# Optimization experiments

Measured on AMD Instinct MI355X. Metric: run time of the kernel, lower is better.

Reference implementation:

```python
import jax, jax.numpy as jnp
import numpy as np

B, N, C, NT = 32, 512, 32, 24   # batch, frames, channels-per-token, tokens
H, DH = 8, 48                   # heads, dim_head (DH % NT == 0 -> CS = 2)
E = H * DH                      # encode_dim = 384
IN = C * NT                     # in_dim = 768
OUT = 768                       # out_dim


def setup_inputs() -> dict:
    key = jax.random.key(0)
    ks = jax.random.split(key, 12)
    s = lambda fan_in: 1.0 / np.sqrt(fan_in)
    return {
        "x": jax.random.normal(ks[0], (B, N, C, NT), dtype=jnp.float32),
        "Wqkv_t": jax.random.uniform(ks[1], (IN, 3 * E), jnp.float32, -s(IN), s(IN)),
        "bqkv_t": jax.random.uniform(ks[2], (3 * E,), jnp.float32, -s(IN), s(IN)),
        "Wqkv_s": jax.random.uniform(ks[3], (IN, 3 * E), jnp.float32, -s(IN), s(IN)),
        "bqkv_s": jax.random.uniform(ks[4], (3 * E,), jnp.float32, -s(IN), s(IN)),
        "Wts": jax.random.uniform(ks[5], (2 * E, 2 * E), jnp.float32, -s(2 * E), s(2 * E)),
        "bts": jax.random.uniform(ks[6], (2 * E,), jnp.float32, -s(2 * E), s(2 * E)),
        "Wfc_t": jax.random.uniform(ks[7], (E, OUT), jnp.float32, -s(E), s(E)),
        "bfc_t": jax.random.uniform(ks[8], (OUT,), jnp.float32, -s(E), s(E)),
        "Wfc_s": jax.random.uniform(ks[9], (E, OUT), jnp.float32, -s(E), s(E)),
        "bfc_s": jax.random.uniform(ks[10], (OUT,), jnp.float32, -s(E), s(E)),
    }


def reference(x, Wqkv_t, bqkv_t, Wqkv_s, bqkv_s, Wts, bts, Wfc_t, bfc_t, Wfc_s, bfc_s):
    b, n, c, nt = x.shape
    cs = DH // nt  # channels per token inside a head (=2)
    xf = x.reshape(b, n, c * nt)                       # (b, n, in_dim)

    # --- temporal attention over the n (frame) axis ---
    qkv_t = (xf @ Wqkv_t + bqkv_t).reshape(b, n, 3, H, DH)
    qkv_t = jnp.transpose(qkv_t, (2, 0, 3, 1, 4))      # (3, b, H, n, DH)
    qt, kt, vt = qkv_t[0], qkv_t[1], qkv_t[2]
    attn_t = jax.nn.softmax(
        jnp.einsum('bhnd,bhmd->bhnm', qt, kt) / jnp.sqrt(jnp.float32(DH)), axis=-1)
    x_t = jnp.einsum('bhnm,bhmd->bnhd', attn_t, vt).reshape(b, n, E)

    # --- spatial attention over the nt (token) axis (note: unscaled, per source) ---
    qkv_s = (xf @ Wqkv_s + bqkv_s).reshape(b, n, 3, H, DH)
    qkv_s = jnp.transpose(qkv_s, (2, 0, 1, 3, 4)).reshape(3, b * n, H, cs, nt)
    qs, ks_, vs = qkv_s[0], qkv_s[1], qkv_s[2]         # (b*n, H, cs, nt)
    attn_s = jax.nn.softmax(jnp.einsum('ghct,ghcu->ghtu', qs, ks_), axis=-1)
    x_s = jnp.einsum('ghtu,ghcu->ghct', attn_s, vs)     # (b*n, H, cs, nt)
    x_s = x_s.reshape(b * n, H, cs * nt).reshape(b, n, E)

    # --- learned gating fusion ---
    alpha = jnp.concatenate([x_t, x_s], axis=-1).mean(axis=1, keepdims=True)  # (b,1,2E)
    alpha = (alpha @ Wts + bts).reshape(b, 1, E, 2)
    alpha = jax.nn.softmax(alpha, axis=-1)
    y = (x_t * alpha[:, :, :, 0]) @ Wfc_t + bfc_t + (x_s * alpha[:, :, :, 1]) @ Wfc_s + bfc_s
    return y  # dropout is identity in inference
```

## Files before the change

### kernel.cpp

```cpp
#include <hip/hip_runtime.h>
#include <hip/hip_bf16.h>


typedef __attribute__((ext_vector_type(8))) short s16x8;
typedef __attribute__((ext_vector_type(4))) float f32x4;

__device__ __forceinline__ float lo2f(uint u) { return __uint_as_float(u << 16); }
__device__ __forceinline__ float hi2f(uint u) { return __uint_as_float(u & 0xffff0000u); }
__device__ __forceinline__ ushort f2bu(float f) {
    union { __hip_bfloat16 h; ushort u; } c; c.h = __float2bfloat16(f); return c.u;
}
__device__ __forceinline__ uint pk2(float a, float b) {
    return (uint)f2bu(a) | ((uint)f2bu(b) << 16);
}
__device__ __forceinline__ void gload16(const void* g, void* l) {
    __builtin_amdgcn_global_load_lds((const __attribute__((address_space(1))) void*)g,
                                     (__attribute__((address_space(3))) void*)l, 16, 0, 0);
}

__global__ __launch_bounds__(256) void convert_bf16(
    const float* __restrict__ in, ushort* __restrict__ out)
{
    const int i = blockIdx.x * 256 + threadIdx.x;
    const float4* p = (const float4*)in + (size_t)i * 2;
    float4 a = p[0], b = p[1];
    uint4 o;
    o.x = pk2(a.x, a.y); o.y = pk2(a.z, a.w);
    o.z = pk2(b.x, b.y); o.w = pk2(b.z, b.w);
    ((uint4*)out)[i] = o;
}

__global__ __launch_bounds__(256) void concat_bias(
    const float* __restrict__ a, const float* __restrict__ b, float* __restrict__ o)
{
    const int i = blockIdx.x * 256 + threadIdx.x;
    o[i] = (i < 1152) ? a[i] : b[i - 1152];
}

__global__ __launch_bounds__(256) void transpose_w(
    const float* __restrict__ W, ushort* __restrict__ Bt,
    int K, int N, int Kt, int koff, int noff)
{
    __shared__ float t[32][33];
    const int k0 = blockIdx.x * 32, n0 = blockIdx.y * 32;
    const int r = threadIdx.x >> 3, cq = threadIdx.x & 7;
    float4 v = *(const float4*)(W + (size_t)(k0 + r) * N + n0 + cq * 4);
    t[r][cq * 4 + 0] = v.x; t[r][cq * 4 + 1] = v.y;
    t[r][cq * 4 + 2] = v.z; t[r][cq * 4 + 3] = v.w;
    __syncthreads();
    ushort4 o;
    o.x = f2bu(t[cq * 4 + 0][r]); o.y = f2bu(t[cq * 4 + 1][r]);
    o.z = f2bu(t[cq * 4 + 2][r]); o.w = f2bu(t[cq * 4 + 3][r]);
    *(ushort4*)(Bt + (size_t)(noff + n0 + r) * Kt + koff + k0 + cq * 4) = o;
}

template<int OUTBF16, int NBIAS>
__global__ __launch_bounds__(256, 2) void gemm128p(
    const ushort* __restrict__ A, const ushort* __restrict__ Bt,
    const float* __restrict__ bias0, const float* __restrict__ bias1,
    void* __restrict__ Cout, int M, int N, int K)
{
    __shared__ ushort smem[32768];
    const int tid = threadIdx.x;
    const int m0 = blockIdx.x * 128;
    const int n0 = blockIdx.y * 128;
    const int lane = tid & 63;
    const int wr = tid >> 7;
    const int wc = (tid >> 6) & 1;
    const int lr = lane & 15;
    const int g = lane >> 4;

    f32x4 acc[4][4];
#pragma unroll
    for (int i = 0; i < 4; ++i)
#pragma unroll
        for (int j = 0; j < 4; ++j) acc[i][j] = (f32x4){0.f, 0.f, 0.f, 0.f};

    int rowT[4], kqs[4];
#pragma unroll
    for (int i = 0; i < 4; ++i) {
        const int task = tid + 256 * i;
        rowT[i] = task >> 3;
        kqs[i] = (task & 7) ^ (rowT[i] & 7);
    }

    auto stage = [&](int buf, int k0) {
        ushort* dA = &smem[buf * 16384];
        ushort* dB = &smem[buf * 16384 + 8192];
#pragma unroll
        for (int i = 0; i < 4; ++i) {
            gload16(A + (size_t)(m0 + rowT[i]) * K + k0 + (kqs[i] << 3),
                    dA + (tid + 256 * i) * 8);
            gload16(Bt + (size_t)(n0 + rowT[i]) * K + k0 + (kqs[i] << 3),
                    dB + (tid + 256 * i) * 8);
        }
    };

    stage(0, 0);
    const int nt = K >> 6;
    for (int t = 0; t < nt; ++t) {
        const int cur = t & 1;
        if (t + 1 < nt) {
            stage(cur ^ 1, (t + 1) << 6);
            asm volatile("s_waitcnt vmcnt(8)" ::: "memory");
        } else {
            asm volatile("s_waitcnt vmcnt(0)" ::: "memory");
        }
        __builtin_amdgcn_sched_barrier(0);
        __builtin_amdgcn_s_barrier();
        __builtin_amdgcn_sched_barrier(0);

        const ushort* As = &smem[cur * 16384];
        const ushort* Bs = &smem[cur * 16384 + 8192];
#pragma unroll
        for (int half = 0; half < 2; ++half) {
            s16x8 af[4], bfv[4];
#pragma unroll
            for (int i = 0; i < 4; ++i) {
                const int row = wr * 64 + 16 * i + lr;
                af[i] = *(const s16x8*)&As[row * 64
                         + (((4 * half + g) ^ (row & 7)) << 3)];
            }
#pragma unroll
            for (int j = 0; j < 4; ++j) {
                const int row = wc * 64 + 16 * j + lr;
                bfv[j] = *(const s16x8*)&Bs[row * 64
                          + (((4 * half + g) ^ (row & 7)) << 3)];
            }
#pragma unroll
            for (int i = 0; i < 4; ++i)
#pragma unroll
                for (int j = 0; j < 4; ++j)
                    acc[i][j] = __builtin_amdgcn_mfma_f32_16x16x32_bf16(
                        af[i], bfv[j], acc[i][j], 0, 0, 0);
        }
        __builtin_amdgcn_sched_barrier(0);
        __builtin_amdgcn_s_barrier();
    }

    const int c0 = n0 + wc * 64 + lr;
    float bsum[4];
#pragma unroll
    for (int j = 0; j < 4; ++j) {
        bsum[j] = bias0[c0 + 16 * j];
        if (NBIAS == 2) bsum[j] += bias1[c0 + 16 * j];
    }
    const int r0 = m0 + wr * 64 + g * 4;
#pragma unroll
    for (int i = 0; i < 4; ++i) {
        const int row = r0 + 16 * i;
#pragma unroll
        for (int j = 0; j < 4; ++j) {
            const int col = c0 + 16 * j;
#pragma unroll
            for (int v = 0; v < 4; ++v) {
                const float val = acc[i][j][v] + bsum[j];
                if (OUTBF16)
                    ((ushort*)Cout)[(size_t)(row + v) * N + col] = f2bu(val);
                else
                    ((float*)Cout)[(size_t)(row + v) * N + col] = val;
            }
        }
    }
}

__global__ __launch_bounds__(256, 4) void attn_temporal(
    const ushort* __restrict__ qkv, ushort* __restrict__ xcat)
{
    const int wg = blockIdx.x;
    const int cx = wg & 7, rx = wg >> 3;
    const int id = ((rx >> 2) << 5) + 4 * cx + (rx & 3);
    const int qt = id & 3;
    const int h = (id >> 2) & 7;
    const int b = id >> 5;

    const int tid = threadIdx.x;
    const int w = tid >> 6;
    const int lane = tid & 63;
    const int lr = lane & 15;
    const int g = lane >> 4;

    __shared__ ushort Ks[64 * 64];
    __shared__ ushort Vt[48 * 64];
    __shared__ ushort Pl[4][32 * 72];
    uint* KsU = (uint*)Ks;
    uint* VtU = (uint*)Vt;

    ((uint4*)Ks)[tid] = make_uint4(0u, 0u, 0u, 0u);
    ((uint4*)Ks)[256 + tid] = make_uint4(0u, 0u, 0u, 0u);
    __syncthreads();

    const uint* qkvu = (const uint*)qkv;
    const int qrow0 = qt * 128 + w * 32;

    s16x8 qf[2][2];
#pragma unroll
    for (int n = 0; n < 2; ++n) {
        const size_t rb = (size_t)(b * 512 + qrow0 + 16 * n + lr) * 2304 + h * 48 + 8 * g;
        qf[n][0] = *(const s16x8*)(qkv + rb);
        qf[n][1] = (g < 2) ? *(const s16x8*)(qkv + rb + 32)
                           : (s16x8){0, 0, 0, 0, 0, 0, 0, 0};
    }

    int p_[3], du_[3];
#pragma unroll
    for (int i = 0; i < 3; ++i) {
        const int idx = tid + 256 * i;
        p_[i] = idx / 24;
        du_[i] = idx % 24;
    }
    uint rk[3][2], rv[3][2];

    auto stage_load = [&](int kv0) {
#pragma unroll
        for (int i = 0; i < 3; ++i) {
            const uint* s0 = qkvu + (size_t)(b * 512 + kv0 + 2 * p_[i]) * 1152
                                  + 192 + h * 24 + du_[i];
            rk[i][0] = s0[0];    rk[i][1] = s0[1152];
            rv[i][0] = s0[192];  rv[i][1] = s0[192 + 1152];
        }
    };
    auto stage_write = [&]() {
#pragma unroll
        for (int i = 0; i < 3; ++i) {
            const int p = p_[i], du = du_[i];
            KsU[(2 * p) * 32 + ((((du >> 2) ^ ((2 * p) & 7)) << 2) | (du & 3))] = rk[i][0];
            KsU[(2 * p + 1) * 32 + ((((du >> 2) ^ ((2 * p + 1) & 7)) << 2) | (du & 3))] = rk[i][1];
            const uint w0 = (rv[i][0] & 0xffffu) | (rv[i][1] << 16);
            const uint w1 = (rv[i][0] >> 16) | (rv[i][1] & 0xffff0000u);
            const int vb = (((p >> 2) ^ (du & 7)) << 2) | (p & 3);
            VtU[(2 * du) * 32 + vb] = w0;
            VtU[(2 * du + 1) * 32 + vb] = w1;
        }
    };

    f32x4 o[2][3];
#pragma unroll
    for (int mq = 0; mq < 2; ++mq)
#pragma unroll
        for (int nd = 0; nd < 3; ++nd) o[mq][nd] = (f32x4){0.f, 0.f, 0.f, 0.f};
    float mrun[2] = {-3.0e38f, -3.0e38f};
    float lsum[2] = {0.f, 0.f};
    float corrv[2];
    const float scale = 0.14433756729740643f;

    stage_load(0);
    stage_write();
    __syncthreads();

    for (int t = 0; t < 8; ++t) {
        if (t < 7) stage_load((t + 1) * 64);

        f32x4 sa[4][2];
#pragma unroll
        for (int m = 0; m < 4; ++m)
#pragma unroll
            for (int n = 0; n < 2; ++n) sa[m][n] = (f32x4){0.f, 0.f, 0.f, 0.f};
#pragma unroll
        for (int ks = 0; ks < 2; ++ks)
#pragma unroll
            for (int m = 0; m < 4; ++m) {
                s16x8 kf = *(const s16x8*)&Ks[(16 * m + lr) * 64
                                              + (((g + 4 * ks) ^ (lr & 7)) << 3)];
#pragma unroll
                for (int n = 0; n < 2; ++n)
                    sa[m][n] = __builtin_amdgcn_mfma_f32_16x16x32_bf16(
                        kf, qf[n][ks], sa[m][n], 0, 0, 0);
            }

#pragma unroll
        for (int n = 0; n < 2; ++n) {
            float tmax = -3.0e38f;
#pragma unroll
            for (int m = 0; m < 4; ++m)
#pragma unroll
                for (int v = 0; v < 4; ++v) tmax = fmaxf(tmax, sa[m][n][v]);
            tmax = fmaxf(tmax, __shfl_xor(tmax, 16));
            tmax = fmaxf(tmax, __shfl_xor(tmax, 32));
            float mnew = fmaxf(mrun[n], tmax * scale);
            float corr = __expf(mrun[n] - mnew);
            mrun[n] = mnew;
            float psum = 0.f;
#pragma unroll
            for (int m = 0; m < 4; ++m) {
                float p0 = __expf(fmaf(sa[m][n][0], scale, -mnew));
                float p1 = __expf(fmaf(sa[m][n][1], scale, -mnew));
                float p2 = __expf(fmaf(sa[m][n][2], scale, -mnew));
                float p3 = __expf(fmaf(sa[m][n][3], scale, -mnew));
                psum += (p0 + p1) + (p2 + p3);
                const int base = (16 * n + lr) * 72 + 16 * m + 4 * g;
                *(uint*)&Pl[w][base] = pk2(p0, p1);
                *(uint*)&Pl[w][base + 2] = pk2(p2, p3);
            }
            psum += __shfl_xor(psum, 16);
            psum += __shfl_xor(psum, 32);
            lsum[n] = lsum[n] * corr + psum;
            corrv[n] = corr;
        }

#pragma unroll
        for (int mq = 0; mq < 2; ++mq)
#pragma unroll
            for (int nd = 0; nd < 3; ++nd)
#pragma unroll
                for (int v = 0; v < 4; ++v) o[mq][nd][v] *= corrv[mq];

#pragma unroll
        for (int ks = 0; ks < 2; ++ks) {
            s16x8 vf[3];
#pragma unroll
            for (int nd = 0; nd < 3; ++nd)
                vf[nd] = *(const s16x8*)&Vt[(16 * nd + lr) * 64
                                            + (((g + 4 * ks) ^ (lr >> 1)) << 3)];
#pragma unroll
            for (int mq = 0; mq < 2; ++mq) {
                s16x8 pf = *(const s16x8*)&Pl[w][(16 * mq + lr) * 72 + 8 * g + 32 * ks];
#pragma unroll
                for (int nd = 0; nd < 3; ++nd)
                    o[mq][nd] = __builtin_amdgcn_mfma_f32_16x16x32_bf16(
                        vf[nd], pf, o[mq][nd], 0, 0, 0);
            }
        }
        __syncthreads();
        if (t < 7) stage_write();
        __syncthreads();
    }

#pragma unroll
    for (int mq = 0; mq < 2; ++mq) {
        const float li = 1.f / lsum[mq];
        const int qrow = qrow0 + 16 * mq + lr;
        ushort* dst = xcat + (size_t)(b * 512 + qrow) * 768 + h * 48;
#pragma unroll
        for (int nd = 0; nd < 3; ++nd) {
            uint2 o2;
            o2.x = pk2(o[mq][nd][0] * li, o[mq][nd][1] * li);
            o2.y = pk2(o[mq][nd][2] * li, o[mq][nd][3] * li);
            *(uint2*)(dst + 16 * nd + 4 * g) = o2;
        }
    }
}

__global__ __launch_bounds__(192) void attn_spatial(
    const ushort* __restrict__ qkv, ushort* __restrict__ xcat)
{
    const int g = blockIdx.x;
    __shared__ float row[1152];
    const uint* qkvu = (const uint*)qkv;
#pragma unroll
    for (int i = 0; i < 3; ++i) {
        int idx = threadIdx.x + 192 * i;
        uint u = qkvu[(size_t)g * 1152 + 576 + idx];
        row[2 * idx] = lo2f(u); row[2 * idx + 1] = hi2f(u);
    }
    __syncthreads();

    const int h = threadIdx.x / 24;
    const int t = threadIdx.x % 24;
    const float* q = &row[h * 48];
    const float* k = &row[384 + h * 48];
    const float* v = &row[768 + h * 48];
    const float q0 = q[t], q1 = q[24 + t];

    float s[24];
    float mx = -3.0e38f;
#pragma unroll
    for (int u = 0; u < 24; ++u) {
        s[u] = q0 * k[u] + q1 * k[24 + u];
        mx = fmaxf(mx, s[u]);
    }
    float l = 0.f;
#pragma unroll
    for (int u = 0; u < 24; ++u) { s[u] = __expf(s[u] - mx); l += s[u]; }
    const float inv = 1.f / l;
    float o0 = 0.f, o1 = 0.f;
#pragma unroll
    for (int u = 0; u < 24; ++u) {
        o0 = fmaf(s[u], v[u], o0);
        o1 = fmaf(s[u], v[24 + u], o1);
    }
    ushort* dst = xcat + (size_t)g * 768 + 384 + h * 48;
    dst[t] = f2bu(o0 * inv);
    dst[24 + t] = f2bu(o1 * inv);
}

__global__ __launch_bounds__(256) void colsum(
    const ushort* __restrict__ xcat, float* __restrict__ partial)
{
    const int b = blockIdx.x, ch = blockIdx.y, part = blockIdx.z;
    const int e = ch * 256 + threadIdx.x;
    const int n0 = part * 64;
    float s = 0.f;
    for (int n = 0; n < 64; ++n)
        s += __uint_as_float((uint)xcat[((size_t)(b * 512 + n0 + n)) * 768 + e] << 16);
    partial[((size_t)(b * 8 + part)) * 768 + e] = s;
}

__global__ __launch_bounds__(256) void alpha_gate(
    const float* __restrict__ partial, const float* __restrict__ Wts,
    const float* __restrict__ bts, float* __restrict__ gate)
{
    const int b = blockIdx.x;
    const int j0 = blockIdx.y * 128;
    __shared__ float av[768];
    __shared__ float psum[2][128];

    for (int i = threadIdx.x; i < 768; i += 256) {
        float s = 0.f;
#pragma unroll
        for (int p = 0; p < 8; ++p)
            s += partial[((size_t)(b * 8 + p)) * 768 + i];
        av[i] = s * (1.0f / 512.0f);
    }
    __syncthreads();

    const int jl = threadIdx.x & 127;
    const int seg = threadIdx.x >> 7;
    const int j = j0 + jl;
    const float* Wp = Wts + (size_t)(seg * 384) * 768 + j;
    const float* avp = av + seg * 384;
    float a0 = 0.f, a1 = 0.f, a2 = 0.f, a3 = 0.f;
    float a4 = 0.f, a5 = 0.f, a6 = 0.f, a7 = 0.f;
#pragma unroll 4
    for (int k = 0; k < 384; k += 8) {
        a0 = fmaf(avp[k + 0], Wp[(size_t)(k + 0) * 768], a0);
        a1 = fmaf(avp[k + 1], Wp[(size_t)(k + 1) * 768], a1);
        a2 = fmaf(avp[k + 2], Wp[(size_t)(k + 2) * 768], a2);
        a3 = fmaf(avp[k + 3], Wp[(size_t)(k + 3) * 768], a3);
        a4 = fmaf(avp[k + 4], Wp[(size_t)(k + 4) * 768], a4);
        a5 = fmaf(avp[k + 5], Wp[(size_t)(k + 5) * 768], a5);
        a6 = fmaf(avp[k + 6], Wp[(size_t)(k + 6) * 768], a6);
        a7 = fmaf(avp[k + 7], Wp[(size_t)(k + 7) * 768], a7);
    }
    psum[seg][jl] = ((a0 + a1) + (a2 + a3)) + ((a4 + a5) + (a6 + a7));
    __syncthreads();

    if (threadIdx.x < 128)
        av[threadIdx.x] = psum[0][threadIdx.x] + psum[1][threadIdx.x]
                        + bts[j0 + threadIdx.x];
    __syncthreads();
    if (threadIdx.x < 64) {
        const int e = (j0 >> 1) + threadIdx.x;
        float x0 = av[2 * threadIdx.x], x1 = av[2 * threadIdx.x + 1];
        float m = fmaxf(x0, x1);
        float e0 = __expf(x0 - m), e1 = __expf(x1 - m);
        float inv = 1.f / (e0 + e1);
        gate[(size_t)b * 768 + e] = e0 * inv;
        gate[(size_t)b * 768 + 384 + e] = e1 * inv;
    }
}

__global__ __launch_bounds__(256) void gate_mul(
    const ushort* __restrict__ xcat, const float* __restrict__ gate,
    ushort* __restrict__ xg)
{
    const int i = blockIdx.x * 256 + threadIdx.x;
    const int m = i / 96;
    const int k = (i % 96) * 8;
    const int b = m >> 9;
    uint4 u = ((const uint4*)xcat)[i];
    const float* g = gate + (size_t)b * 768 + k;
    float4 g0 = *(const float4*)g;
    float4 g1 = *(const float4*)(g + 4);
    uint4 o;
    o.x = pk2(lo2f(u.x) * g0.x, hi2f(u.x) * g0.y);
    o.y = pk2(lo2f(u.y) * g0.z, hi2f(u.y) * g0.w);
    o.z = pk2(lo2f(u.z) * g1.x, hi2f(u.z) * g1.y);
    o.w = pk2(lo2f(u.w) * g1.z, hi2f(u.w) * g1.w);
    ((uint4*)xg)[i] = o;
}

extern "C" void kernel_launch(void* const* d_in, const int* in_sizes, int n_in,
                              void* d_out, int out_size, void* d_ws, size_t ws_size,
                              hipStream_t stream)
{
    const float* x      = (const float*)d_in[0];
    const float* Wqkv_t = (const float*)d_in[1];
    const float* bqkv_t = (const float*)d_in[2];
    const float* Wqkv_s = (const float*)d_in[3];
    const float* bqkv_s = (const float*)d_in[4];
    const float* Wts    = (const float*)d_in[5];
    const float* bts    = (const float*)d_in[6];
    const float* Wfc_t  = (const float*)d_in[7];
    const float* bfc_t  = (const float*)d_in[8];
    const float* Wfc_s  = (const float*)d_in[9];
    const float* bfc_s  = (const float*)d_in[10];
    float* out = (float*)d_out;

    char* w = (char*)d_ws;
    ushort* qkv2   = (ushort*)(w);
    ushort* xg     = qkv2;
    ushort* xcat   = (ushort*)(w + 75497472);
    ushort* xb     = (ushort*)(w + 100663296);
    ushort* wbuf   = (ushort*)(w + 125829120);
    ushort* wbuf2  = (ushort*)(w + 129368064);
    float*  partial= (float*)(w + 130547712);
    float*  gate   = (float*)(w + 131334144);
    float*  bias2  = (float*)(w + 131432448);

    const dim3 blk256(256);

    convert_bf16<<<dim3(6144), blk256, 0, stream>>>(x, xb);
    concat_bias<<<dim3(9), blk256, 0, stream>>>(bqkv_t, bqkv_s, bias2);
    transpose_w<<<dim3(24, 36), blk256, 0, stream>>>(Wqkv_t, wbuf, 768, 1152, 768, 0, 0);
    transpose_w<<<dim3(24, 36), blk256, 0, stream>>>(Wqkv_s, wbuf, 768, 1152, 768, 0, 1152);

    gemm128p<1, 1><<<dim3(128, 18), blk256, 0, stream>>>(
        xb, wbuf, bias2, nullptr, qkv2, 16384, 2304, 768);

    attn_temporal<<<dim3(1024), blk256, 0, stream>>>(qkv2, xcat);
    attn_spatial<<<dim3(16384), dim3(192), 0, stream>>>(qkv2, xcat);

    colsum<<<dim3(32, 3, 8), blk256, 0, stream>>>(xcat, partial);
    alpha_gate<<<dim3(32, 6), blk256, 0, stream>>>(partial, Wts, bts, gate);
    gate_mul<<<dim3(6144), blk256, 0, stream>>>(xcat, gate, xg);

    transpose_w<<<dim3(12, 24), blk256, 0, stream>>>(Wfc_t, wbuf2, 384, 768, 768, 0, 0);
    transpose_w<<<dim3(12, 24), blk256, 0, stream>>>(Wfc_s, wbuf2, 384, 768, 768, 384, 0);
    gemm128p<0, 2><<<dim3(128, 6), blk256, 0, stream>>>(
        xg, wbuf2, bfc_t, bfc_s, out, 16384, 768, 768);
}
```

Measured before the change: 200.5 us.

## Enlarge GEMM tiles to 256x256 with 512 threads and XCD-aware block mapping

Replaces the 128x128 GEMM with a 256x256 tile using 8 waves (each computing 128x64) and 64KB of double-buffered LDS. It also remaps the 1D grid so that each XCD gets a contiguous range of M row-blocks, which should improve L2 reuse of A. The goal is higher arithmetic intensity per LDS load and fewer global reloads. The cost is fewer blocks (576 and 192 on 256 CUs, giving wave-quantization imbalance) and higher register pressure from 32 accumulators per wave, with only one block per CU.

```diff
diff --git a/kernel.cpp b/kernel.cpp
--- a/kernel.cpp
+++ b/kernel.cpp
@@ -54,45 +54,51 @@
     *(ushort4*)(Bt + (size_t)(noff + n0 + r) * Kt + koff + k0 + cq * 4) = o;
 }
 
-template<int OUTBF16, int NBIAS>
-__global__ __launch_bounds__(256, 2) void gemm128p(
+template<int OUTBF16, int NBIAS, int NBT>
+__global__ __launch_bounds__(512, 1) void gemm256p(
     const ushort* __restrict__ A, const ushort* __restrict__ Bt,
     const float* __restrict__ bias0, const float* __restrict__ bias1,
     void* __restrict__ Cout, int M, int N, int K)
 {
-    __shared__ ushort smem[32768];
+    __shared__ ushort smem[65536];
     const int tid = threadIdx.x;
-    const int m0 = blockIdx.x * 128;
-    const int n0 = blockIdx.y * 128;
+
+    const int id = blockIdx.x;
+    const int xcd = id & 7;
+    const int j = id >> 3;
+    const int m0 = (xcd * ((M >> 8) >> 3) + j / NBT) << 8;
+    const int n0 = (j % NBT) << 8;
+
     const int lane = tid & 63;
-    const int wr = tid >> 7;
-    const int wc = (tid >> 6) & 1;
+    const int wid = tid >> 6;
+    const int wr = wid >> 2;
+    const int wc = wid & 3;
     const int lr = lane & 15;
     const int g = lane >> 4;
 
-    f32x4 acc[4][4];
-#pragma unroll
-    for (int i = 0; i < 4; ++i)
-#pragma unroll
-        for (int j = 0; j < 4; ++j) acc[i][j] = (f32x4){0.f, 0.f, 0.f, 0.f};
+    f32x4 acc[8][4];
+#pragma unroll
+    for (int i = 0; i < 8; ++i)
+#pragma unroll
+        for (int jj = 0; jj < 4; ++jj) acc[i][jj] = (f32x4){0.f, 0.f, 0.f, 0.f};
 
     int rowT[4], kqs[4];
 #pragma unroll
     for (int i = 0; i < 4; ++i) {
-        const int task = tid + 256 * i;
+        const int task = tid + 512 * i;
         rowT[i] = task >> 3;
         kqs[i] = (task & 7) ^ (rowT[i] & 7);
     }
 
     auto stage = [&](int buf, int k0) {
-        ushort* dA = &smem[buf * 16384];
-        ushort* dB = &smem[buf * 16384 + 8192];
+        ushort* dA = &smem[buf * 32768];
+        ushort* dB = &smem[buf * 32768 + 16384];
 #pragma unroll
         for (int i = 0; i < 4; ++i) {
             gload16(A + (size_t)(m0 + rowT[i]) * K + k0 + (kqs[i] << 3),
-                    dA + (tid + 256 * i) * 8);
+                    dA + (tid + 512 * i) * 8);
             gload16(Bt + (size_t)(n0 + rowT[i]) * K + k0 + (kqs[i] << 3),
-                    dB + (tid + 256 * i) * 8);
+                    dB + (tid + 512 * i) * 8);
         }
     };
 
@@ -110,29 +116,29 @@
         __builtin_amdgcn_s_barrier();
         __builtin_amdgcn_sched_barrier(0);
 
-        const ushort* As = &smem[cur * 16384];
-        const ushort* Bs = &smem[cur * 16384 + 8192];
+        const ushort* As = &smem[cur * 32768];
+        const ushort* Bs = &smem[cur * 32768 + 16384];
 #pragma unroll
         for (int half = 0; half < 2; ++half) {
-            s16x8 af[4], bfv[4];
-#pragma unroll
-            for (int i = 0; i < 4; ++i) {
-                const int row = wr * 64 + 16 * i + lr;
+            s16x8 af[8], bfv[4];
+#pragma unroll
+            for (int i = 0; i < 8; ++i) {
+                const int row = wr * 128 + 16 * i + lr;
                 af[i] = *(const s16x8*)&As[row * 64
                          + (((4 * half + g) ^ (row & 7)) << 3)];
             }
 #pragma unroll
-            for (int j = 0; j < 4; ++j) {
-                const int row = wc * 64 + 16 * j + lr;
-                bfv[j] = *(const s16x8*)&Bs[row * 64
-                          + (((4 * half + g) ^ (row & 7)) << 3)];
+            for (int jj = 0; jj < 4; ++jj) {
+                const int row = wc * 64 + 16 * jj + lr;
+                bfv[jj] = *(const s16x8*)&Bs[row * 64
+                           + (((4 * half + g) ^ (row & 7)) << 3)];
             }
 #pragma unroll
-            for (int i = 0; i < 4; ++i)
-#pragma unroll
-                for (int j = 0; j < 4; ++j)
-                    acc[i][j] = __builtin_amdgcn_mfma_f32_16x16x32_bf16(
-                        af[i], bfv[j], acc[i][j], 0, 0, 0);
+            for (int i = 0; i < 8; ++i)
+#pragma unroll
+                for (int jj = 0; jj < 4; ++jj)
+                    acc[i][jj] = __builtin_amdgcn_mfma_f32_16x16x32_bf16(
+                        af[i], bfv[jj], acc[i][jj], 0, 0, 0);
         }
         __builtin_amdgcn_sched_barrier(0);
         __builtin_amdgcn_s_barrier();
@@ -141,20 +147,20 @@
     const int c0 = n0 + wc * 64 + lr;
     float bsum[4];
 #pragma unroll
-    for (int j = 0; j < 4; ++j) {
-        bsum[j] = bias0[c0 + 16 * j];
-        if (NBIAS == 2) bsum[j] += bias1[c0 + 16 * j];
-    }
-    const int r0 = m0 + wr * 64 + g * 4;
-#pragma unroll
-    for (int i = 0; i < 4; ++i) {
+    for (int jj = 0; jj < 4; ++jj) {
+        bsum[jj] = bias0[c0 + 16 * jj];
+        if (NBIAS == 2) bsum[jj] += bias1[c0 + 16 * jj];
+    }
+    const int r0 = m0 + wr * 128 + g * 4;
+#pragma unroll
+    for (int i = 0; i < 8; ++i) {
         const int row = r0 + 16 * i;
 #pragma unroll
-        for (int j = 0; j < 4; ++j) {
-            const int col = c0 + 16 * j;
+        for (int jj = 0; jj < 4; ++jj) {
+            const int col = c0 + 16 * jj;
 #pragma unroll
             for (int v = 0; v < 4; ++v) {
-                const float val = acc[i][j][v] + bsum[j];
+                const float val = acc[i][jj][v] + bsum[jj];
                 if (OUTBF16)
                     ((ushort*)Cout)[(size_t)(row + v) * N + col] = f2bu(val);
                 else
@@ -505,7 +511,7 @@
     transpose_w<<<dim3(24, 36), blk256, 0, stream>>>(Wqkv_t, wbuf, 768, 1152, 768, 0, 0);
     transpose_w<<<dim3(24, 36), blk256, 0, stream>>>(Wqkv_s, wbuf, 768, 1152, 768, 0, 1152);
 
-    gemm128p<1, 1><<<dim3(128, 18), blk256, 0, stream>>>(
+    gemm256p<1, 1, 9><<<dim3(576), dim3(512), 0, stream>>>(
         xb, wbuf, bias2, nullptr, qkv2, 16384, 2304, 768);
 
     attn_temporal<<<dim3(1024), blk256, 0, stream>>>(qkv2, xcat);
@@ -517,6 +523,6 @@
 
     transpose_w<<<dim3(12, 24), blk256, 0, stream>>>(Wfc_t, wbuf2, 384, 768, 768, 0, 0);
     transpose_w<<<dim3(12, 24), blk256, 0, stream>>>(Wfc_s, wbuf2, 384, 768, 768, 384, 0);
-    gemm128p<0, 2><<<dim3(128, 6), blk256, 0, stream>>>(
+    gemm256p<0, 2, 3><<<dim3(192), dim3(512), 0, stream>>>(
         xg, wbuf2, bfc_t, bfc_s, out, 16384, 768, 768);
 }
```

After: 214.7 us. +7.1%, slower.

## Fuse gate multiply into final GEMM A-load and remap GEMM blocks per XCD

Applied to the files above, without the earlier changes.

Removes the separate gate_mul kernel. The final GEMM now loads xcat rows through registers, scales them by the per-batch gate held in shared memory, and writes them into LDS, which saves a full read and write of the 16384x768 bf16 intermediate. Both GEMMs also use a 1D grid remapped so that each XCD handles a contiguous range of M tiles with all N tiles, aiming at better L2 reuse of A rows. The A path changes from async global-to-LDS loads to register loads with explicit waitcnt, which could reduce latency hiding in the final GEMM.

```diff
diff --git a/kernel.cpp b/kernel.cpp
--- a/kernel.cpp
+++ b/kernel.cpp
@@ -54,7 +54,7 @@
     *(ushort4*)(Bt + (size_t)(noff + n0 + r) * Kt + koff + k0 + cq * 4) = o;
 }
 
-template<int OUTBF16, int NBIAS>
+template<int OUTBF16, int NBIAS, int NBT>
 __global__ __launch_bounds__(256, 2) void gemm128p(
     const ushort* __restrict__ A, const ushort* __restrict__ Bt,
     const float* __restrict__ bias0, const float* __restrict__ bias1,
@@ -62,8 +62,13 @@
 {
     __shared__ ushort smem[32768];
     const int tid = threadIdx.x;
-    const int m0 = blockIdx.x * 128;
-    const int n0 = blockIdx.y * 128;
+
+    const int id = blockIdx.x;
+    const int xcd = id & 7;
+    const int rr = id >> 3;
+    const int m0 = ((xcd * ((M >> 7) >> 3)) + rr / NBT) << 7;
+    const int n0 = (rr % NBT) << 7;
+
     const int lane = tid & 63;
     const int wr = tid >> 7;
     const int wc = (tid >> 6) & 1;
@@ -160,6 +165,138 @@
                 else
                     ((float*)Cout)[(size_t)(row + v) * N + col] = val;
             }
+        }
+    }
+}
+
+template<int NBT>
+__global__ __launch_bounds__(256, 2) void gemm128g(
+    const ushort* __restrict__ A, const ushort* __restrict__ Bt,
+    const float* __restrict__ bias0, const float* __restrict__ bias1,
+    const float* __restrict__ gate, float* __restrict__ Cout,
+    int M, int N, int K)
+{
+    __shared__ ushort smem[32768];
+    __shared__ float gs[768];
+    const int tid = threadIdx.x;
+    const int id = blockIdx.x;
+    const int xcd = id & 7;
+    const int rr = id >> 3;
+    const int m0 = ((xcd * ((M >> 7) >> 3)) + rr / NBT) << 7;
+    const int n0 = (rr % NBT) << 7;
+
+    const int lane = tid & 63;
+    const int wr = tid >> 7;
+    const int wc = (tid >> 6) & 1;
+    const int lr = lane & 15;
+    const int g = lane >> 4;
+
+    f32x4 acc[4][4];
+#pragma unroll
+    for (int i = 0; i < 4; ++i)
+#pragma unroll
+        for (int j = 0; j < 4; ++j) acc[i][j] = (f32x4){0.f, 0.f, 0.f, 0.f};
+
+    int rowT[4], kqs[4];
+#pragma unroll
+    for (int i = 0; i < 4; ++i) {
+        const int task = tid + 256 * i;
+        rowT[i] = task >> 3;
+        kqs[i] = (task & 7) ^ (rowT[i] & 7);
+    }
+
+    uint4 va[4];
+    auto stageB = [&](int buf, int k0) {
+        ushort* dB = &smem[buf * 16384 + 8192];
+#pragma unroll
+        for (int i = 0; i < 4; ++i)
+            gload16(Bt + (size_t)(n0 + rowT[i]) * K + k0 + (kqs[i] << 3),
+                    dB + (tid + 256 * i) * 8);
+    };
+    auto loadA = [&](int k0) {
+#pragma unroll
+        for (int i = 0; i < 4; ++i)
+            va[i] = *(const uint4*)(A + (size_t)(m0 + rowT[i]) * K + k0
+                                    + (kqs[i] << 3));
+    };
+    auto writeA = [&](int buf, int k0) {
+        ushort* dA = &smem[buf * 16384];
+#pragma unroll
+        for (int i = 0; i < 4; ++i) {
+            const float* gp = &gs[k0 + (kqs[i] << 3)];
+            uint4 o;
+            o.x = pk2(lo2f(va[i].x) * gp[0], hi2f(va[i].x) * gp[1]);
+            o.y = pk2(lo2f(va[i].y) * gp[2], hi2f(va[i].y) * gp[3]);
+            o.z = pk2(lo2f(va[i].z) * gp[4], hi2f(va[i].z) * gp[5]);
+            o.w = pk2(lo2f(va[i].w) * gp[6], hi2f(va[i].w) * gp[7]);
+            *(uint4*)&dA[(tid + 256 * i) * 8] = o;
+        }
+    };
+
+    const float* gsrc = gate + (size_t)(m0 >> 9) * 768;
+    stageB(0, 0);
+    loadA(0);
+    for (int i = tid; i < 768; i += 256) gs[i] = gsrc[i];
+    __syncthreads();
+    writeA(0, 0);
+    __syncthreads();
+
+    const int nt = K >> 6;
+    for (int t = 0; t < nt; ++t) {
+        const int cur = t & 1;
+        const bool pf = (t + 1) < nt;
+        if (pf) { stageB(cur ^ 1, (t + 1) << 6); loadA((t + 1) << 6); }
+
+        const ushort* As = &smem[cur * 16384];
+        const ushort* Bs = &smem[cur * 16384 + 8192];
+#pragma unroll
+        for (int half = 0; half < 2; ++half) {
+            s16x8 af[4], bfv[4];
+#pragma unroll
+            for (int i = 0; i < 4; ++i) {
+                const int row = wr * 64 + 16 * i + lr;
+                af[i] = *(const s16x8*)&As[row * 64
+                         + (((4 * half + g) ^ (row & 7)) << 3)];
+            }
+#pragma unroll
+            for (int j = 0; j < 4; ++j) {
+                const int row = wc * 64 + 16 * j + lr;
+                bfv[j] = *(const s16x8*)&Bs[row * 64
+                          + (((4 * half + g) ^ (row & 7)) << 3)];
+            }
+#pragma unroll
+            for (int i = 0; i < 4; ++i)
+#pragma unroll
+                for (int j = 0; j < 4; ++j)
+                    acc[i][j] = __builtin_amdgcn_mfma_f32_16x16x32_bf16(
+                        af[i], bfv[j], acc[i][j], 0, 0, 0);
+        }
+        if (pf) {
+            __builtin_amdgcn_sched_barrier(0);
+            asm volatile("s_waitcnt vmcnt(0)" ::: "memory");
+            __builtin_amdgcn_sched_barrier(0);
+            writeA(cur ^ 1, (t + 1) << 6);
+            asm volatile("s_waitcnt lgkmcnt(0)" ::: "memory");
+            __builtin_amdgcn_sched_barrier(0);
+            __builtin_amdgcn_s_barrier();
+        }
+    }
+
+    const int c0 = n0 + wc * 64 + lr;
+    float bsum[4];
+#pragma unroll
+    for (int j = 0; j < 4; ++j)
+        bsum[j] = bias0[c0 + 16 * j] + bias1[c0 + 16 * j];
+    const int r0 = m0 + wr * 64 + g * 4;
+#pragma unroll
+    for (int i = 0; i < 4; ++i) {
+        const int row = r0 + 16 * i;
+#pragma unroll
+        for (int j = 0; j < 4; ++j) {
+            const int col = c0 + 16 * j;
+#pragma unroll
+            for (int v = 0; v < 4; ++v)
+                Cout[(size_t)(row + v) * N + col] = acc[i][j][v] + bsum[j];
         }
     }
 }
@@ -450,26 +587,6 @@
     }
 }
 
-__global__ __launch_bounds__(256) void gate_mul(
-    const ushort* __restrict__ xcat, const float* __restrict__ gate,
-    ushort* __restrict__ xg)
-{
-    const int i = blockIdx.x * 256 + threadIdx.x;
-    const int m = i / 96;
-    const int k = (i % 96) * 8;
-    const int b = m >> 9;
-    uint4 u = ((const uint4*)xcat)[i];
-    const float* g = gate + (size_t)b * 768 + k;
-    float4 g0 = *(const float4*)g;
-    float4 g1 = *(const float4*)(g + 4);
-    uint4 o;
-    o.x = pk2(lo2f(u.x) * g0.x, hi2f(u.x) * g0.y);
-    o.y = pk2(lo2f(u.y) * g0.z, hi2f(u.y) * g0.w);
-    o.z = pk2(lo2f(u.z) * g1.x, hi2f(u.z) * g1.y);
-    o.w = pk2(lo2f(u.w) * g1.z, hi2f(u.w) * g1.w);
-    ((uint4*)xg)[i] = o;
-}
-
 extern "C" void kernel_launch(void* const* d_in, const int* in_sizes, int n_in,
                               void* d_out, int out_size, void* d_ws, size_t ws_size,
                               hipStream_t stream)
@@ -489,7 +606,6 @@
 
     char* w = (char*)d_ws;
     ushort* qkv2   = (ushort*)(w);
-    ushort* xg     = qkv2;
     ushort* xcat   = (ushort*)(w + 75497472);
     ushort* xb     = (ushort*)(w + 100663296);
     ushort* wbuf   = (ushort*)(w + 125829120);
@@ -505,7 +621,7 @@
     transpose_w<<<dim3(24, 36), blk256, 0, stream>>>(Wqkv_t, wbuf, 768, 1152, 768, 0, 0);
     transpose_w<<<dim3(24, 36), blk256, 0, stream>>>(Wqkv_s, wbuf, 768, 1152, 768, 0, 1152);
 
-    gemm128p<1, 1><<<dim3(128, 18), blk256, 0, stream>>>(
+    gemm128p<1, 1, 18><<<dim3(2304), blk256, 0, stream>>>(
         xb, wbuf, bias2, nullptr, qkv2, 16384, 2304, 768);
 
     attn_temporal<<<dim3(1024), blk256, 0, stream>>>(qkv2, xcat);
@@ -513,10 +629,9 @@
 
     colsum<<<dim3(32, 3, 8), blk256, 0, stream>>>(xcat, partial);
     alpha_gate<<<dim3(32, 6), blk256, 0, stream>>>(partial, Wts, bts, gate);
-    gate_mul<<<dim3(6144), blk256, 0, stream>>>(xcat, gate, xg);
 
     transpose_w<<<dim3(12, 24), blk256, 0, stream>>>(Wfc_t, wbuf2, 384, 768, 768, 0, 0);
     transpose_w<<<dim3(12, 24), blk256, 0, stream>>>(Wfc_s, wbuf2, 384, 768, 768, 384, 0);
-    gemm128p<0, 2><<<dim3(128, 6), blk256, 0, stream>>>(
-        xg, wbuf2, bfc_t, bfc_s, out, 16384, 768, 768);
-}
+    gemm128g<6><<<dim3(768), blk256, 0, stream>>>(
+        xcat, wbuf2, bfc_t, bfc_s, gate, out, 16384, 768, 768);
+}
```

New measurement: 212.1 us. 1.06x slower.

## Pre-shuffle weights into MFMA fragment layout and load B directly to registers

Applied to the files above, without the earlier changes.

Replaces the weight transpose kernel with a shuffle that writes bf16 weights in per-lane MFMA fragment order, so the GEMM loads B fragments straight from global memory into registers instead of staging them through LDS. This halves LDS use and LDS traffic per tile and drops the B-side LDS reads, at the cost of per-wave global loads of B that rely on L2 reuse. It also adds s_setprio around MFMA blocks in the GEMM and temporal attention to favour matrix-issue waves.

```diff
diff --git a/kernel.cpp b/kernel.cpp
--- a/kernel.cpp
+++ b/kernel.cpp
@@ -37,38 +37,38 @@
     o[i] = (i < 1152) ? a[i] : b[i - 1152];
 }
 
-__global__ __launch_bounds__(256) void transpose_w(
-    const float* __restrict__ W, ushort* __restrict__ Bt,
-    int K, int N, int Kt, int koff, int noff)
-{
-    __shared__ float t[32][33];
-    const int k0 = blockIdx.x * 32, n0 = blockIdx.y * 32;
-    const int r = threadIdx.x >> 3, cq = threadIdx.x & 7;
-    float4 v = *(const float4*)(W + (size_t)(k0 + r) * N + n0 + cq * 4);
-    t[r][cq * 4 + 0] = v.x; t[r][cq * 4 + 1] = v.y;
-    t[r][cq * 4 + 2] = v.z; t[r][cq * 4 + 3] = v.w;
-    __syncthreads();
-    ushort4 o;
-    o.x = f2bu(t[cq * 4 + 0][r]); o.y = f2bu(t[cq * 4 + 1][r]);
-    o.z = f2bu(t[cq * 4 + 2][r]); o.w = f2bu(t[cq * 4 + 3][r]);
-    *(ushort4*)(Bt + (size_t)(noff + n0 + r) * Kt + koff + k0 + cq * 4) = o;
+__global__ __launch_bounds__(64) void shuffle_w(
+    const float* __restrict__ W, ushort* __restrict__ Bf,
+    int N, int KC, int kc_off, int nt_off)
+{
+    const int kc = blockIdx.x, nt = blockIdx.y;
+    const int l = threadIdx.x;
+    const int n = nt * 16 + (l & 15);
+    const int k0 = kc * 32 + (l >> 4) * 8;
+    ushort v[8];
+#pragma unroll
+    for (int e = 0; e < 8; ++e)
+        v[e] = f2bu(W[(size_t)(k0 + e) * N + n]);
+    ushort* dst = Bf + (((size_t)(nt_off + nt) * KC + kc_off + kc) << 9) + l * 8;
+    *(uint4*)dst = *(const uint4*)v;
 }
 
 template<int OUTBF16, int NBIAS>
-__global__ __launch_bounds__(256, 2) void gemm128p(
-    const ushort* __restrict__ A, const ushort* __restrict__ Bt,
+__global__ __launch_bounds__(256, 2) void gemm128f(
+    const ushort* __restrict__ A, const ushort* __restrict__ Bf,
     const float* __restrict__ bias0, const float* __restrict__ bias1,
     void* __restrict__ Cout, int M, int N, int K)
 {
-    __shared__ ushort smem[32768];
+    __shared__ ushort As2[16384];
     const int tid = threadIdx.x;
-    const int m0 = blockIdx.x * 128;
-    const int n0 = blockIdx.y * 128;
+    const int m0 = blockIdx.x << 7;
+    const int n0 = blockIdx.y << 7;
     const int lane = tid & 63;
     const int wr = tid >> 7;
     const int wc = (tid >> 6) & 1;
     const int lr = lane & 15;
     const int g = lane >> 4;
+    const int KC = K >> 5;
 
     f32x4 acc[4][4];
 #pragma unroll
@@ -83,26 +83,33 @@
         rowT[i] = task >> 3;
         kqs[i] = (task & 7) ^ (rowT[i] & 7);
     }
-
-    auto stage = [&](int buf, int k0) {
-        ushort* dA = &smem[buf * 16384];
-        ushort* dB = &smem[buf * 16384 + 8192];
-#pragma unroll
-        for (int i = 0; i < 4; ++i) {
+    auto stageA = [&](int buf, int k0) {
+        ushort* dA = &As2[buf * 8192];
+#pragma unroll
+        for (int i = 0; i < 4; ++i)
             gload16(A + (size_t)(m0 + rowT[i]) * K + k0 + (kqs[i] << 3),
                     dA + (tid + 256 * i) * 8);
-            gload16(Bt + (size_t)(n0 + rowT[i]) * K + k0 + (kqs[i] << 3),
-                    dB + (tid + 256 * i) * 8);
-        }
     };
 
-    stage(0, 0);
+    const ushort* bbase = Bf + (((size_t)((n0 >> 4) + wc * 4) * KC) << 9) + lane * 8;
+    s16x8 bs[2][4];
+    auto loadB = [&](int t) {
+#pragma unroll
+        for (int half = 0; half < 2; ++half)
+#pragma unroll
+            for (int j = 0; j < 4; ++j)
+                bs[half][j] = *(const s16x8*)(bbase
+                    + (((size_t)j * KC + 2 * t + half) << 9));
+    };
+
+    stageA(0, 0);
     const int nt = K >> 6;
     for (int t = 0; t < nt; ++t) {
         const int cur = t & 1;
+        loadB(t);
         if (t + 1 < nt) {
-            stage(cur ^ 1, (t + 1) << 6);
-            asm volatile("s_waitcnt vmcnt(8)" ::: "memory");
+            stageA(cur ^ 1, (t + 1) << 6);
+            asm volatile("s_waitcnt vmcnt(4)" ::: "memory");
         } else {
             asm volatile("s_waitcnt vmcnt(0)" ::: "memory");
         }
@@ -110,29 +117,24 @@
         __builtin_amdgcn_s_barrier();
         __builtin_amdgcn_sched_barrier(0);
 
-        const ushort* As = &smem[cur * 16384];
-        const ushort* Bs = &smem[cur * 16384 + 8192];
+        const ushort* Asc = &As2[cur * 8192];
 #pragma unroll
         for (int half = 0; half < 2; ++half) {
-            s16x8 af[4], bfv[4];
+            s16x8 af[4];
 #pragma unroll
             for (int i = 0; i < 4; ++i) {
                 const int row = wr * 64 + 16 * i + lr;
-                af[i] = *(const s16x8*)&As[row * 64
+                af[i] = *(const s16x8*)&Asc[row * 64
                          + (((4 * half + g) ^ (row & 7)) << 3)];
             }
-#pragma unroll
-            for (int j = 0; j < 4; ++j) {
-                const int row = wc * 64 + 16 * j + lr;
-                bfv[j] = *(const s16x8*)&Bs[row * 64
-                          + (((4 * half + g) ^ (row & 7)) << 3)];
-            }
+            __builtin_amdgcn_s_setprio(1);
 #pragma unroll
             for (int i = 0; i < 4; ++i)
 #pragma unroll
                 for (int j = 0; j < 4; ++j)
                     acc[i][j] = __builtin_amdgcn_mfma_f32_16x16x32_bf16(
-                        af[i], bfv[j], acc[i][j], 0, 0, 0);
+                        af[i], bs[half][j], acc[i][j], 0, 0, 0);
+            __builtin_amdgcn_s_setprio(0);
         }
         __builtin_amdgcn_sched_barrier(0);
         __builtin_amdgcn_s_barrier();
@@ -256,6 +258,7 @@
         for (int m = 0; m < 4; ++m)
 #pragma unroll
             for (int n = 0; n < 2; ++n) sa[m][n] = (f32x4){0.f, 0.f, 0.f, 0.f};
+        __builtin_amdgcn_s_setprio(1);
 #pragma unroll
         for (int ks = 0; ks < 2; ++ks)
 #pragma unroll
@@ -267,6 +270,7 @@
                     sa[m][n] = __builtin_amdgcn_mfma_f32_16x16x32_bf16(
                         kf, qf[n][ks], sa[m][n], 0, 0, 0);
             }
+        __builtin_amdgcn_s_setprio(0);
 
 #pragma unroll
         for (int n = 0; n < 2; ++n) {
@@ -305,6 +309,7 @@
 #pragma unroll
                 for (int v = 0; v < 4; ++v) o[mq][nd][v] *= corrv[mq];
 
+        __builtin_amdgcn_s_setprio(1);
 #pragma unroll
         for (int ks = 0; ks < 2; ++ks) {
             s16x8 vf[3];
@@ -321,6 +326,7 @@
                         vf[nd], pf, o[mq][nd], 0, 0, 0);
             }
         }
+        __builtin_amdgcn_s_setprio(0);
         __syncthreads();
         if (t < 7) stage_write();
         __syncthreads();
@@ -502,10 +508,10 @@
 
     convert_bf16<<<dim3(6144), blk256, 0, stream>>>(x, xb);
     concat_bias<<<dim3(9), blk256, 0, stream>>>(bqkv_t, bqkv_s, bias2);
-    transpose_w<<<dim3(24, 36), blk256, 0, stream>>>(Wqkv_t, wbuf, 768, 1152, 768, 0, 0);
-    transpose_w<<<dim3(24, 36), blk256, 0, stream>>>(Wqkv_s, wbuf, 768, 1152, 768, 0, 1152);
-
-    gemm128p<1, 1><<<dim3(128, 18), blk256, 0, stream>>>(
+    shuffle_w<<<dim3(24, 72), dim3(64), 0, stream>>>(Wqkv_t, wbuf, 1152, 24, 0, 0);
+    shuffle_w<<<dim3(24, 72), dim3(64), 0, stream>>>(Wqkv_s, wbuf, 1152, 24, 0, 72);
+
+    gemm128f<1, 1><<<dim3(128, 18), blk256, 0, stream>>>(
         xb, wbuf, bias2, nullptr, qkv2, 16384, 2304, 768);
 
     attn_temporal<<<dim3(1024), blk256, 0, stream>>>(qkv2, xcat);
@@ -515,8 +521,8 @@
     alpha_gate<<<dim3(32, 6), blk256, 0, stream>>>(partial, Wts, bts, gate);
     gate_mul<<<dim3(6144), blk256, 0, stream>>>(xcat, gate, xg);
 
-    transpose_w<<<dim3(12, 24), blk256, 0, stream>>>(Wfc_t, wbuf2, 384, 768, 768, 0, 0);
-    transpose_w<<<dim3(12, 24), blk256, 0, stream>>>(Wfc_s, wbuf2, 384, 768, 768, 384, 0);
-    gemm128p<0, 2><<<dim3(128, 6), blk256, 0, stream>>>(
+    shuffle_w<<<dim3(12, 48), dim3(64), 0, stream>>>(Wfc_t, wbuf2, 768, 24, 0, 0);
+    shuffle_w<<<dim3(12, 48), dim3(64), 0, stream>>>(Wfc_s, wbuf2, 768, 24, 12, 0);
+    gemm128f<0, 2><<<dim3(128, 6), blk256, 0, stream>>>(
         xg, wbuf2, bfc_t, bfc_s, out, 16384, 768, 768);
 }
```

Measured after the change: 201.0 us. About the same (+0.3%).
